# Kernel optimization log

Measured on AMD Instinct MI355X. Metric: run time of the kernel, lower is better.

Reference implementation:

```python
import jax, jax.numpy as jnp
import numpy as np

IN_FEATURES = 4096
OUT_FEATURES = 4096
TOKENS = 8192


def setup_inputs() -> dict:
    key = jax.random.key(0)
    k_in, k_w = jax.random.split(key)
    x = jax.random.normal(k_in, (TOKENS, IN_FEATURES), dtype=jnp.float32)
    # xavier_uniform: U(-a, a) with a = sqrt(6 / (fan_in + fan_out))
    a = float(np.sqrt(6.0 / (IN_FEATURES + OUT_FEATURES)))
    weight = jax.random.uniform(k_w, (OUT_FEATURES, IN_FEATURES), dtype=jnp.float32,
                                minval=-a, maxval=a)
    return {"input": x, "weight": weight}


def reference(input, weight):
    # Ternarize: keep sign where |w| > mean(|w|), else 0
    abs_w = jnp.abs(weight)
    abs_mean = jnp.mean(abs_w)
    w_ternary = jnp.where(abs_w > abs_mean, jnp.sign(weight), jnp.zeros_like(weight))
    # F.linear: x @ W^T   -> [tokens, out_features]
    return input @ w_ternary.T
```

## Files before the change

kernel.cpp:

```cpp
#include <hip/hip_runtime.h>

#define M_TOK 8192
#define N_OUT 4096
#define K_IN  4096
#define NT    (K_IN / 64)

typedef _Float16 f16x8 __attribute__((ext_vector_type(8)));
typedef _Float16 f16x4 __attribute__((ext_vector_type(4)));
typedef float    f32x4 __attribute__((ext_vector_type(4)));


__global__ void k_absmean_partial(const float* __restrict__ w, double* __restrict__ partials) {
    const int n4 = (N_OUT * K_IN) / 4;
    double s = 0.0;
    for (int i = blockIdx.x * blockDim.x + threadIdx.x; i < n4; i += gridDim.x * blockDim.x) {
        float4 v = reinterpret_cast<const float4*>(w)[i];
        s += (double)fabsf(v.x);
        s += (double)fabsf(v.y);
        s += (double)fabsf(v.z);
        s += (double)fabsf(v.w);
    }
    #pragma unroll
    for (int off = 32; off > 0; off >>= 1) s += __shfl_down(s, off, 64);
    __shared__ double sm[4];
    if ((threadIdx.x & 63) == 0) sm[threadIdx.x >> 6] = s;
    __syncthreads();
    if (threadIdx.x == 0) partials[blockIdx.x] = sm[0] + sm[1] + sm[2] + sm[3];
}

__global__ void k_absmean_final(const double* __restrict__ partials, float* __restrict__ meanp) {
    double s = 0.0;
    for (int i = threadIdx.x; i < 1024; i += 256) s += partials[i];
    #pragma unroll
    for (int off = 32; off > 0; off >>= 1) s += __shfl_down(s, off, 64);
    __shared__ double sm[4];
    if ((threadIdx.x & 63) == 0) sm[threadIdx.x >> 6] = s;
    __syncthreads();
    if (threadIdx.x == 0)
        *meanp = (float)((sm[0] + sm[1] + sm[2] + sm[3]) / (double)((long long)N_OUT * K_IN));
}


__global__ void k_ternarize(const float* __restrict__ w, const float* __restrict__ meanp,
                            _Float16* __restrict__ wt) {
    const float t = *meanp;
    const int n4 = (N_OUT * K_IN) / 4;
    for (int i = blockIdx.x * blockDim.x + threadIdx.x; i < n4; i += gridDim.x * blockDim.x) {
        float4 v = reinterpret_cast<const float4*>(w)[i];
        f16x4 r;
        r[0] = (_Float16)((fabsf(v.x) > t) ? ((v.x > 0.f) ? 1.f : -1.f) : 0.f);
        r[1] = (_Float16)((fabsf(v.y) > t) ? ((v.y > 0.f) ? 1.f : -1.f) : 0.f);
        r[2] = (_Float16)((fabsf(v.z) > t) ? ((v.z > 0.f) ? 1.f : -1.f) : 0.f);
        r[3] = (_Float16)((fabsf(v.w) > t) ? ((v.w > 0.f) ? 1.f : -1.f) : 0.f);
        reinterpret_cast<f16x4*>(wt)[i] = r;
    }
}

__global__ void k_cvt_x(const float* __restrict__ x, _Float16* __restrict__ xh) {
    const int n4 = (M_TOK * K_IN) / 4;
    for (int i = blockIdx.x * blockDim.x + threadIdx.x; i < n4; i += gridDim.x * blockDim.x) {
        float4 v = reinterpret_cast<const float4*>(x)[i];
        f16x4 r;
        r[0] = (_Float16)v.x;
        r[1] = (_Float16)v.y;
        r[2] = (_Float16)v.z;
        r[3] = (_Float16)v.w;
        reinterpret_cast<f16x4*>(xh)[i] = r;
    }
}


__device__ __forceinline__ void g2lds16(const _Float16* g, _Float16* l) {
    __builtin_amdgcn_global_load_lds(
        (const __attribute__((address_space(1))) unsigned int*)g,
        (__attribute__((address_space(3))) unsigned int*)l, 16, 0, 0);
}

__global__ __launch_bounds__(512, 2) void k_gemm(const _Float16* __restrict__ A,
                                                 const _Float16* __restrict__ B,
                                                 float* __restrict__ C) {
    __shared__ _Float16 lds[65536];
    const int tid  = threadIdx.x;
    const int lane = tid & 63;
    const int wid  = tid >> 6;
    const int wm   = wid >> 2;
    const int wn   = wid & 3;
    const int lr   = lane & 15;
    const int lg   = lane >> 4;
    const int xv   = lr & 7;
    const int bm   = blockIdx.y, bn = blockIdx.x;

    const _Float16* gA = A + (size_t)bm * 256 * K_IN;
    const _Float16* gB = B + (size_t)bn * 256 * K_IN;

    const int srow = tid >> 3;
    const int scol = ((tid & 7) ^ (srow & 7)) << 3;
    const int swb  = wid * 512;

#define STAGE(gb, matOff, half, kt, buf) do {                                         \
    g2lds16((gb) + (size_t)((half) * 128 + srow) * K_IN + (kt) * 64 + scol,           \
            &lds[(buf) * 32768 + (matOff) + (half) * 8192 + swb]);                    \
    g2lds16((gb) + (size_t)((half) * 128 + 64 + srow) * K_IN + (kt) * 64 + scol,      \
            &lds[(buf) * 32768 + (matOff) + (half) * 8192 + 4096 + swb]);             \
} while (0)

    f32x4 acc[4][4][2];
    const f32x4 vz = {0.f, 0.f, 0.f, 0.f};
    #pragma unroll
    for (int q = 0; q < 4; ++q)
        #pragma unroll
        for (int mf = 0; mf < 4; ++mf)
            #pragma unroll
            for (int nf = 0; nf < 2; ++nf) acc[q][mf][nf] = vz;

    STAGE(gA, 0,     0, 0, 0);
    STAGE(gB, 16384, 1, 0, 0);
    STAGE(gB, 16384, 0, 0, 0);
    STAGE(gA, 0,     1, 0, 0);
    STAGE(gA, 0,     0, 1, 1);
    STAGE(gB, 16384, 1, 1, 1);
    asm volatile("s_waitcnt vmcnt(4)" ::: "memory");
    __builtin_amdgcn_s_barrier();

    const int arow = wm * 64 + lr;
    const int brow = wn * 32 + lr;

#define LDA(qm, cb) do {                                                              \
    _Pragma("unroll") for (int mf = 0; mf < 4; ++mf)                                  \
    _Pragma("unroll") for (int kk = 0; kk < 2; ++kk)                                  \
        af[mf][kk] = *reinterpret_cast<const f16x8*>(                                 \
            &lds[(cb) + (qm) * 8192 + (arow + mf * 16) * 64 + ((kk * 4 + lg) ^ xv) * 8]); \
} while (0)
#define LDB(qn, cb) do {                                                              \
    _Pragma("unroll") for (int nf = 0; nf < 2; ++nf)                                  \
    _Pragma("unroll") for (int kk = 0; kk < 2; ++kk)                                  \
        bf[nf][kk] = *reinterpret_cast<const f16x8*>(                                 \
            &lds[(cb) + 16384 + (qn) * 8192 + (brow + nf * 16) * 64 + ((kk * 4 + lg) ^ xv) * 8]); \
} while (0)
#define MFMAQ(q) do {                                                                 \
    __builtin_amdgcn_s_setprio(1);                                                    \
    _Pragma("unroll") for (int mf = 0; mf < 4; ++mf)                                  \
    _Pragma("unroll") for (int nf = 0; nf < 2; ++nf)                                  \
    _Pragma("unroll") for (int kk = 0; kk < 2; ++kk)                                  \
        acc[q][mf][nf] = __builtin_amdgcn_mfma_f32_16x16x32_f16(                      \
            af[mf][kk], bf[nf][kk], acc[q][mf][nf], 0, 0, 0);                         \
    __builtin_amdgcn_s_setprio(0);                                                    \
} while (0)

    for (int t = 0; t < NT; ++t) {
        const int cur = t & 1;
        const int cb  = cur * 32768;
        const int nxt = cur ^ 1;
        f16x8 af[4][2], bf[2][2];

        LDA(0, cb); LDB(0, cb);
        if (t + 1 < NT) STAGE(gB, 16384, 0, t + 1, nxt);
        __builtin_amdgcn_s_barrier();
        asm volatile("s_waitcnt lgkmcnt(0)");
        MFMAQ(0);
        __builtin_amdgcn_s_barrier();

        LDB(1, cb);
        if (t + 1 < NT) STAGE(gA, 0, 1, t + 1, nxt);
        __builtin_amdgcn_s_barrier();
        asm volatile("s_waitcnt lgkmcnt(0)");
        MFMAQ(1);
        __builtin_amdgcn_s_barrier();

        LDA(1, cb);
        if (t + 2 < NT) STAGE(gA, 0, 0, t + 2, cur);
        __builtin_amdgcn_s_barrier();
        asm volatile("s_waitcnt lgkmcnt(0)");
        MFMAQ(2);
        __builtin_amdgcn_s_barrier();

        LDB(0, cb);
        if (t + 2 < NT) STAGE(gB, 16384, 1, t + 2, cur);
        __builtin_amdgcn_s_barrier();
        asm volatile("s_waitcnt lgkmcnt(0)");
        MFMAQ(3);
        if (t < NT - 2) asm volatile("s_waitcnt vmcnt(4)" ::: "memory");
        else            asm volatile("s_waitcnt vmcnt(0)" ::: "memory");
        __builtin_amdgcn_s_barrier();
    }

    const int qmv[4] = {0, 0, 1, 1}, qnv[4] = {0, 1, 1, 0};
    #pragma unroll
    for (int q = 0; q < 4; ++q)
        #pragma unroll
        for (int mf = 0; mf < 4; ++mf)
            #pragma unroll
            for (int nf = 0; nf < 2; ++nf)
                #pragma unroll
                for (int j = 0; j < 4; ++j) {
                    const int row = bm * 256 + qmv[q] * 128 + wm * 64 + mf * 16 + lg * 4 + j;
                    const int col = bn * 256 + qnv[q] * 128 + wn * 32 + nf * 16 + lr;
                    C[(size_t)row * N_OUT + col] = acc[q][mf][nf][j];
                }
#undef STAGE
#undef LDA
#undef LDB
#undef MFMAQ
}


extern "C" void kernel_launch(void* const* d_in, const int* in_sizes, int n_in,
                              void* d_out, int out_size, void* d_ws, size_t ws_size,
                              hipStream_t stream) {
    const float* x   = (const float*)d_in[0];
    const float* wgt = (const float*)d_in[1];
    float* out = (float*)d_out;

    double*   partials = (double*)d_ws;
    float*    meanp    = (float*)((char*)d_ws + 8192);
    _Float16* Xh       = (_Float16*)((char*)d_ws + 16384);
    _Float16* Wh       = Xh + (size_t)M_TOK * K_IN;

    k_absmean_partial<<<1024, 256, 0, stream>>>(wgt, partials);
    k_absmean_final<<<1, 256, 0, stream>>>(partials, meanp);
    k_ternarize<<<2048, 256, 0, stream>>>(wgt, meanp, Wh);
    k_cvt_x<<<2048, 256, 0, stream>>>(x, Xh);

    dim3 grid(N_OUT / 256, M_TOK / 256);
    k_gemm<<<grid, 512, 0, stream>>>(Xh, Wh, out);
}
```

Measured before the change: 486.9 us.

## Double-buffer LDS fragment registers to cut barriers in GEMM main loop

The GEMM inner loop is restructured to keep two sets of A and B fragment registers, so LDS reads for the next quadrant and next tile are issued ahead of the MFMAs that use the current ones. This drops most of the per-quadrant barriers and explicit lgkmcnt waits, leaving two barriers per K tile. The ternarize and x-conversion kernels are also merged into one launch to save a kernel launch. The change raises register pressure under launch_bounds(512,2) and leans on the compiler to insert correct LDS waits, which risks spills or subtle ordering hazards with the async global-to-LDS stages.

```diff
diff --git a/kernel.cpp b/kernel.cpp
--- a/kernel.cpp
+++ b/kernel.cpp
@@ -41,24 +41,23 @@
 }
 
 
-__global__ void k_ternarize(const float* __restrict__ w, const float* __restrict__ meanp,
-                            _Float16* __restrict__ wt) {
+__global__ void k_prep(const float* __restrict__ w, const float* __restrict__ x,
+                       const float* __restrict__ meanp,
+                       _Float16* __restrict__ wh, _Float16* __restrict__ xh) {
     const float t = *meanp;
-    const int n4 = (N_OUT * K_IN) / 4;
-    for (int i = blockIdx.x * blockDim.x + threadIdx.x; i < n4; i += gridDim.x * blockDim.x) {
+    const int stride = gridDim.x * blockDim.x;
+    const int nw4 = (N_OUT * K_IN) / 4;
+    for (int i = blockIdx.x * blockDim.x + threadIdx.x; i < nw4; i += stride) {
         float4 v = reinterpret_cast<const float4*>(w)[i];
         f16x4 r;
         r[0] = (_Float16)((fabsf(v.x) > t) ? ((v.x > 0.f) ? 1.f : -1.f) : 0.f);
         r[1] = (_Float16)((fabsf(v.y) > t) ? ((v.y > 0.f) ? 1.f : -1.f) : 0.f);
         r[2] = (_Float16)((fabsf(v.z) > t) ? ((v.z > 0.f) ? 1.f : -1.f) : 0.f);
         r[3] = (_Float16)((fabsf(v.w) > t) ? ((v.w > 0.f) ? 1.f : -1.f) : 0.f);
-        reinterpret_cast<f16x4*>(wt)[i] = r;
-    }
-}
-
-__global__ void k_cvt_x(const float* __restrict__ x, _Float16* __restrict__ xh) {
-    const int n4 = (M_TOK * K_IN) / 4;
-    for (int i = blockIdx.x * blockDim.x + threadIdx.x; i < n4; i += gridDim.x * blockDim.x) {
+        reinterpret_cast<f16x4*>(wh)[i] = r;
+    }
+    const int nx4 = (M_TOK * K_IN) / 4;
+    for (int i = blockIdx.x * blockDim.x + threadIdx.x; i < nx4; i += stride) {
         float4 v = reinterpret_cast<const float4*>(x)[i];
         f16x4 r;
         r[0] = (_Float16)v.x;
@@ -75,6 +74,10 @@
         (const __attribute__((address_space(1))) unsigned int*)g,
         (__attribute__((address_space(3))) unsigned int*)l, 16, 0, 0);
 }
+
+#define BAR() do { asm volatile("" ::: "memory"); \
+                   __builtin_amdgcn_s_barrier();  \
+                   asm volatile("" ::: "memory"); } while (0)
 
 __global__ __launch_bounds__(512, 2) void k_gemm(const _Float16* __restrict__ A,
                                                  const _Float16* __restrict__ B,
@@ -104,6 +107,35 @@
             &lds[(buf) * 32768 + (matOff) + (half) * 8192 + 4096 + swb]);             \
 } while (0)
 
+    const int arow = wm * 64 + lr;
+    const int brow = wn * 32 + lr;
+    const int ka0  = (lg ^ xv) * 8;
+    const int ka1  = ((4 + lg) ^ xv) * 8;
+
+#define RD_A(dst, qm, cb0) do {                                                       \
+    _Pragma("unroll") for (int mf = 0; mf < 4; ++mf) {                                \
+        const _Float16* p_ = &lds[(cb0) + (qm) * 8192 + (arow + mf * 16) * 64];       \
+        dst[mf][0] = *reinterpret_cast<const f16x8*>(p_ + ka0);                       \
+        dst[mf][1] = *reinterpret_cast<const f16x8*>(p_ + ka1);                       \
+    }                                                                                 \
+} while (0)
+#define RD_B(dst, qn, cb0) do {                                                       \
+    _Pragma("unroll") for (int nf = 0; nf < 2; ++nf) {                                \
+        const _Float16* p_ = &lds[(cb0) + 16384 + (qn) * 8192 + (brow + nf * 16) * 64]; \
+        dst[nf][0] = *reinterpret_cast<const f16x8*>(p_ + ka0);                       \
+        dst[nf][1] = *reinterpret_cast<const f16x8*>(p_ + ka1);                       \
+    }                                                                                 \
+} while (0)
+#define MFMAQ(q, afx, bfx) do {                                                       \
+    __builtin_amdgcn_s_setprio(1);                                                    \
+    _Pragma("unroll") for (int mf = 0; mf < 4; ++mf)                                  \
+    _Pragma("unroll") for (int nf = 0; nf < 2; ++nf)                                  \
+    _Pragma("unroll") for (int kk = 0; kk < 2; ++kk)                                  \
+        acc[q][mf][nf] = __builtin_amdgcn_mfma_f32_16x16x32_f16(                      \
+            afx[mf][kk], bfx[nf][kk], acc[q][mf][nf], 0, 0, 0);                       \
+    __builtin_amdgcn_s_setprio(0);                                                    \
+} while (0)
+
     f32x4 acc[4][4][2];
     const f32x4 vz = {0.f, 0.f, 0.f, 0.f};
     #pragma unroll
@@ -112,6 +144,8 @@
         for (int mf = 0; mf < 4; ++mf)
             #pragma unroll
             for (int nf = 0; nf < 2; ++nf) acc[q][mf][nf] = vz;
+
+    f16x8 af0[4][2], af1[4][2], bf0[2][2], bf1[2][2];
 
     STAGE(gA, 0,     0, 0, 0);
     STAGE(gB, 16384, 1, 0, 0);
@@ -120,68 +154,34 @@
     STAGE(gA, 0,     0, 1, 1);
     STAGE(gB, 16384, 1, 1, 1);
     asm volatile("s_waitcnt vmcnt(4)" ::: "memory");
-    __builtin_amdgcn_s_barrier();
-
-    const int arow = wm * 64 + lr;
-    const int brow = wn * 32 + lr;
-
-#define LDA(qm, cb) do {                                                              \
-    _Pragma("unroll") for (int mf = 0; mf < 4; ++mf)                                  \
-    _Pragma("unroll") for (int kk = 0; kk < 2; ++kk)                                  \
-        af[mf][kk] = *reinterpret_cast<const f16x8*>(                                 \
-            &lds[(cb) + (qm) * 8192 + (arow + mf * 16) * 64 + ((kk * 4 + lg) ^ xv) * 8]); \
-} while (0)
-#define LDB(qn, cb) do {                                                              \
-    _Pragma("unroll") for (int nf = 0; nf < 2; ++nf)                                  \
-    _Pragma("unroll") for (int kk = 0; kk < 2; ++kk)                                  \
-        bf[nf][kk] = *reinterpret_cast<const f16x8*>(                                 \
-            &lds[(cb) + 16384 + (qn) * 8192 + (brow + nf * 16) * 64 + ((kk * 4 + lg) ^ xv) * 8]); \
-} while (0)
-#define MFMAQ(q) do {                                                                 \
-    __builtin_amdgcn_s_setprio(1);                                                    \
-    _Pragma("unroll") for (int mf = 0; mf < 4; ++mf)                                  \
-    _Pragma("unroll") for (int nf = 0; nf < 2; ++nf)                                  \
-    _Pragma("unroll") for (int kk = 0; kk < 2; ++kk)                                  \
-        acc[q][mf][nf] = __builtin_amdgcn_mfma_f32_16x16x32_f16(                      \
-            af[mf][kk], bf[nf][kk], acc[q][mf][nf], 0, 0, 0);                         \
-    __builtin_amdgcn_s_setprio(0);                                                    \
-} while (0)
+    BAR();
+    RD_A(af0, 0, 0);
 
     for (int t = 0; t < NT; ++t) {
         const int cur = t & 1;
         const int cb  = cur * 32768;
         const int nxt = cur ^ 1;
-        f16x8 af[4][2], bf[2][2];
-
-        LDA(0, cb); LDB(0, cb);
+        const int nb  = nxt * 32768;
+
         if (t + 1 < NT) STAGE(gB, 16384, 0, t + 1, nxt);
-        __builtin_amdgcn_s_barrier();
-        asm volatile("s_waitcnt lgkmcnt(0)");
-        MFMAQ(0);
-        __builtin_amdgcn_s_barrier();
-
-        LDB(1, cb);
+        RD_B(bf0, 0, cb);
+        RD_B(bf1, 1, cb);
+        MFMAQ(0, af0, bf0);
+
         if (t + 1 < NT) STAGE(gA, 0, 1, t + 1, nxt);
-        __builtin_amdgcn_s_barrier();
-        asm volatile("s_waitcnt lgkmcnt(0)");
-        MFMAQ(1);
-        __builtin_amdgcn_s_barrier();
-
-        LDA(1, cb);
+        RD_A(af1, 1, cb);
+        MFMAQ(1, af0, bf1);
+        BAR();
+
         if (t + 2 < NT) STAGE(gA, 0, 0, t + 2, cur);
-        __builtin_amdgcn_s_barrier();
-        asm volatile("s_waitcnt lgkmcnt(0)");
-        MFMAQ(2);
-        __builtin_amdgcn_s_barrier();
-
-        LDB(0, cb);
+        MFMAQ(2, af1, bf1);
+
         if (t + 2 < NT) STAGE(gB, 16384, 1, t + 2, cur);
-        __builtin_amdgcn_s_barrier();
-        asm volatile("s_waitcnt lgkmcnt(0)");
-        MFMAQ(3);
         if (t < NT - 2) asm volatile("s_waitcnt vmcnt(4)" ::: "memory");
         else            asm volatile("s_waitcnt vmcnt(0)" ::: "memory");
-        __builtin_amdgcn_s_barrier();
+        BAR();
+        if (t + 1 < NT) RD_A(af0, 0, nb);
+        MFMAQ(3, af1, bf0);
     }
 
     const int qmv[4] = {0, 0, 1, 1}, qnv[4] = {0, 1, 1, 0};
@@ -198,8 +198,8 @@
                     C[(size_t)row * N_OUT + col] = acc[q][mf][nf][j];
                 }
 #undef STAGE
-#undef LDA
-#undef LDB
+#undef RD_A
+#undef RD_B
 #undef MFMAQ
 }
 
@@ -218,8 +218,7 @@
 
     k_absmean_partial<<<1024, 256, 0, stream>>>(wgt, partials);
     k_absmean_final<<<1, 256, 0, stream>>>(partials, meanp);
-    k_ternarize<<<2048, 256, 0, stream>>>(wgt, meanp, Wh);
-    k_cvt_x<<<2048, 256, 0, stream>>>(x, Xh);
+    k_prep<<<2048, 256, 0, stream>>>(wgt, x, meanp, Wh, Xh);
 
     dim3 grid(N_OUT / 256, M_TOK / 256);
     k_gemm<<<grid, 512, 0, stream>>>(Xh, Wh, out);
```

After: 478.6 us. About the same (-1.7%).
